# Optimization experiments

Measured on AMD Instinct MI355X. Metric: run time of the kernel, lower is better.

The kernel has to match this reference:

```python
import jax, jax.numpy as jnp
import numpy as np

BN_EPS = 1e-5

def setup_inputs() -> dict:
    key = jax.random.key(0)
    ks = jax.random.split(key, 16)
    B, n, m, C1, C2 = 16, 4096, 1024, 128, 256
    Cin, H1, H2 = C1 + C2, 256, 128  # mlp = [384, 256, 128]
    inp = {
        "unknown": jax.random.normal(ks[0], (B, n, 3), jnp.float32),
        "known": jax.random.normal(ks[1], (B, m, 3), jnp.float32),
        "unknow_feats": jax.random.normal(ks[2], (B, n, C1), jnp.float32),
        "known_feats": jax.random.normal(ks[3], (B, m, C2), jnp.float32),
        # layer 1: 1x1 conv (Cin->H1) + BN (eval stats) + ReLU
        "W1": jax.random.normal(ks[4], (H1, Cin), jnp.float32) * 0.05,
        "b1": jnp.zeros((H1,), jnp.float32),
        "g1": jnp.ones((H1,), jnp.float32),
        "bt1": jnp.zeros((H1,), jnp.float32),
        "mu1": jax.random.normal(ks[5], (H1,), jnp.float32) * 0.1,
        "v1": jax.random.uniform(ks[6], (H1,), jnp.float32, 0.5, 1.5),
        # layer 2: 1x1 conv (H1->H2) + BN + ReLU
        "W2": jax.random.normal(ks[7], (H2, H1), jnp.float32) * 0.05,
        "b2": jnp.zeros((H2,), jnp.float32),
        "g2": jnp.ones((H2,), jnp.float32),
        "bt2": jnp.zeros((H2,), jnp.float32),
        "mu2": jax.random.normal(ks[8], (H2,), jnp.float32) * 0.1,
        "v2": jax.random.uniform(ks[9], (H2,), jnp.float32, 0.5, 1.5),
    }
    return inp

def _fp_forward(unknown, known, unknow_feats, known_feats,
                W1, b1, g1, bt1, mu1, v1,
                W2, b2, g2, bt2, mu2, v2):
    # --- three_nn: brute-force k=3 nearest neighbors (squared distances) ---
    # d2: (B, n, m)
    d2 = jnp.sum((unknown[:, :, None, :] - known[:, None, :, :]) ** 2, axis=-1)
    neg_dist, idx = jax.lax.top_k(-d2, 3)          # (B, n, 3)
    dist = -neg_dist + 1e-10
    dist_recip = 1.0 / dist
    weight = dist_recip / jnp.sum(dist_recip, axis=2, keepdims=True)  # (B, n, 3)
    # --- three_interpolate: inverse-distance weighted gather ---
    feats_nn = jax.vmap(lambda f, i: f[i])(known_feats, idx)  # (B, n, 3, C2)
    interpolated = jnp.einsum('bnkc,bnk->bnc', feats_nn, weight)
    x = jnp.concatenate([interpolated, unknow_feats], axis=-1)  # (B, n, C1+C2)
    # --- SharedMLP: 1x1 conv + BN(eval) + ReLU, twice ---
    for (W, b, g, bt, mu, v) in ((W1, b1, g1, bt1, mu1, v1),
                                 (W2, b2, g2, bt2, mu2, v2)):
        x = jnp.einsum('bnc,oc->bno', x, W) + b
        x = (x - mu) * (g * jax.lax.rsqrt(v + BN_EPS)) + bt
        x = jax.nn.relu(x)
    return x  # (B, n, mlp[-1])

def reference(unknown, known, unknow_feats, known_feats,
              W1, b1, g1, bt1, mu1, v1,
              W2, b2, g2, bt2, mu2, v2):
    return _fp_forward(unknown, known, unknow_feats, known_feats,
                       W1, b1, g1, bt1, mu1, v1,
                       W2, b2, g2, bt2, mu2, v2)
```

## Files before the change

### kernel.cpp

```cpp
#include <hip/hip_runtime.h>

typedef float f32x4 __attribute__((ext_vector_type(4)));
typedef __bf16 bf16x8 __attribute__((ext_vector_type(8)));

#define BN_EPS 1e-5f

__device__ __forceinline__ unsigned short f2bf(float x) {
  union { float f; unsigned u; } v; v.f = x;
  unsigned r = v.u + 0x7fffu + ((v.u >> 16) & 1u);
  return (unsigned short)(r >> 16);
}

__global__ void prep_kernel(const float* __restrict__ W1, const float* __restrict__ b1,
                            const float* __restrict__ g1, const float* __restrict__ bt1,
                            const float* __restrict__ mu1, const float* __restrict__ v1,
                            const float* __restrict__ W2, const float* __restrict__ b2,
                            const float* __restrict__ g2, const float* __restrict__ bt2,
                            const float* __restrict__ mu2, const float* __restrict__ v2,
                            unsigned short* __restrict__ W1b, unsigned short* __restrict__ W2b,
                            float* __restrict__ bias1, float* __restrict__ bias2) {
  int tid = blockIdx.x * 256 + threadIdx.x;
  if (tid < 98304) {
    int o = tid / 384;
    float s = g1[o] * rsqrtf(v1[o] + BN_EPS);
    W1b[tid] = f2bf(W1[tid] * s);
    if (tid < 256) bias1[tid] = (b1[tid] - mu1[tid]) * (g1[tid] * rsqrtf(v1[tid] + BN_EPS)) + bt1[tid];
  } else if (tid < 98304 + 32768) {
    int t = tid - 98304;
    int o = t / 256;
    float s = g2[o] * rsqrtf(v2[o] + BN_EPS);
    W2b[t] = f2bf(W2[t] * s);
    if (t < 128) bias2[t] = (b2[t] - mu2[t]) * (g2[t] * rsqrtf(v2[t] + BN_EPS)) + bt2[t];
  }
}

__global__ __launch_bounds__(256, 2)
void fp_fused_kernel(const float* __restrict__ unknown, const float* __restrict__ known,
                     const float* __restrict__ unknow_feats, const float* __restrict__ known_feats,
                     const unsigned short* __restrict__ W1b, const unsigned short* __restrict__ W2b,
                     const float* __restrict__ bias1, const float* __restrict__ bias2,
                     float* __restrict__ out) {
  __shared__ float kxyz[3072];
  __shared__ float sd[64 * 12];
  __shared__ int   si[64 * 12];
  __shared__ float w_s[64 * 3];
  __shared__ int   i_s[64 * 3];
  __shared__ __align__(16) unsigned char xbuf[64 * 768];

  int bid = blockIdx.x;
  int swz = ((bid & 7) << 7) | (bid >> 3);
  int b   = swz >> 6;
  int i0  = (swz & 63) << 6;

  int tid = threadIdx.x;
  int l = tid & 63;
  int q = tid >> 6;

  for (int t = tid; t < 3072; t += 256) kxyz[t] = known[b * 3072 + t];

  int pi = i0 + l;
  float ux = unknown[(b * 4096 + pi) * 3 + 0];
  float uy = unknown[(b * 4096 + pi) * 3 + 1];
  float uz = unknown[(b * 4096 + pi) * 3 + 2];
  __syncthreads();

  float d0 = 3.0e38f, d1 = 3.0e38f, d2 = 3.0e38f;
  int   j0 = 0, j1 = 0, j2 = 0;
  int jbase = q << 8;
  for (int jj = 0; jj < 256; ++jj) {
    int j = jbase + jj;
    float dx = ux - kxyz[j * 3 + 0];
    float dy = uy - kxyz[j * 3 + 1];
    float dz = uz - kxyz[j * 3 + 2];
    float d = dx * dx + dy * dy + dz * dz;
    bool c2 = d < d2, c1 = d < d1, c0 = d < d0;
    d2 = c1 ? d1 : (c2 ? d : d2);  j2 = c1 ? j1 : (c2 ? j : j2);
    d1 = c0 ? d0 : (c1 ? d : d1);  j1 = c0 ? j0 : (c1 ? j : j1);
    d0 = c0 ? d : d0;              j0 = c0 ? j : j0;
  }
  int sb = l * 12 + q * 3;
  sd[sb] = d0; sd[sb + 1] = d1; sd[sb + 2] = d2;
  si[sb] = j0; si[sb + 1] = j1; si[sb + 2] = j2;
  __syncthreads();

  if (tid < 64) {
    float m0 = 3.0e38f, m1 = 3.0e38f, m2 = 3.0e38f;
    int   n0 = 0, n1 = 0, n2 = 0;
    for (int e = 0; e < 12; ++e) {
      float d = sd[tid * 12 + e]; int j = si[tid * 12 + e];
      bool c2 = d < m2, c1 = d < m1, c0 = d < m0;
      m2 = c1 ? m1 : (c2 ? d : m2);  n2 = c1 ? n1 : (c2 ? j : n2);
      m1 = c0 ? m0 : (c1 ? d : m1);  n1 = c0 ? n0 : (c1 ? j : n1);
      m0 = c0 ? d : m0;              n0 = c0 ? j : n0;
    }
    float r0 = 1.0f / (m0 + 1e-10f);
    float r1 = 1.0f / (m1 + 1e-10f);
    float r2 = 1.0f / (m2 + 1e-10f);
    float rs = 1.0f / (r0 + r1 + r2);
    w_s[tid * 3 + 0] = r0 * rs; i_s[tid * 3 + 0] = n0;
    w_s[tid * 3 + 1] = r1 * rs; i_s[tid * 3 + 1] = n1;
    w_s[tid * 3 + 2] = r2 * rs; i_s[tid * 3 + 2] = n2;
  }
  __syncthreads();

  {
    int pp = tid >> 6;
    int cq = tid & 63;
    const float4* kf = (const float4*)(known_feats + (size_t)b * 1024 * 256);
    for (int po = 0; po < 16; ++po) {
      int p = po * 4 + pp;
      int ia = i_s[p * 3 + 0], ib = i_s[p * 3 + 1], ic = i_s[p * 3 + 2];
      float wa = w_s[p * 3 + 0], wb = w_s[p * 3 + 1], wc = w_s[p * 3 + 2];
      float4 va = kf[ia * 64 + cq];
      float4 vb = kf[ib * 64 + cq];
      float4 vc = kf[ic * 64 + cq];
      ushort4 h;
      h.x = f2bf(wa * va.x + wb * vb.x + wc * vc.x);
      h.y = f2bf(wa * va.y + wb * vb.y + wc * vc.y);
      h.z = f2bf(wa * va.z + wb * vb.z + wc * vc.z);
      h.w = f2bf(wa * va.w + wb * vb.w + wc * vc.w);
      int byte = p * 768 + cq * 8;
      byte ^= (p & 7) << 4;
      *(ushort4*)(xbuf + byte) = h;
    }
  }
  {
    int pp = tid >> 5;
    int cq = tid & 31;
    const float4* uf = (const float4*)(unknow_feats + ((size_t)b * 4096 + i0) * 128);
    for (int po = 0; po < 8; ++po) {
      int p = po * 8 + pp;
      float4 v = uf[p * 32 + cq];
      ushort4 h;
      h.x = f2bf(v.x); h.y = f2bf(v.y); h.z = f2bf(v.z); h.w = f2bf(v.w);
      int byte = p * 768 + 512 + cq * 8;
      byte ^= (p & 7) << 4;
      *(ushort4*)(xbuf + byte) = h;
    }
  }
  __syncthreads();

  int lr = l & 15;
  int lk = l >> 4;
  f32x4 acc[4][4];
  #pragma unroll
  for (int m = 0; m < 4; ++m)
    #pragma unroll
    for (int n = 0; n < 4; ++n) acc[m][n] = (f32x4){0.f, 0.f, 0.f, 0.f};

  for (int kk = 0; kk < 12; ++kk) {
    int kb = kk * 32 + lk * 8;
    bf16x8 a[4];
    #pragma unroll
    for (int m = 0; m < 4; ++m) {
      int row = m * 16 + lr;
      int byte = row * 768 + kb * 2;
      byte ^= (row & 7) << 4;
      a[m] = *(const bf16x8*)(xbuf + byte);
    }
    #pragma unroll
    for (int n = 0; n < 4; ++n) {
      int wr = q * 64 + n * 16 + lr;
      bf16x8 bb = *(const bf16x8*)(W1b + wr * 384 + kb);
      #pragma unroll
      for (int m = 0; m < 4; ++m)
        acc[m][n] = __builtin_amdgcn_mfma_f32_16x16x32_bf16(a[m], bb, acc[m][n], 0, 0, 0);
    }
  }

  float bs1[4];
  #pragma unroll
  for (int n = 0; n < 4; ++n) bs1[n] = bias1[q * 64 + n * 16 + lr];

  __syncthreads();
  #pragma unroll
  for (int m = 0; m < 4; ++m)
    #pragma unroll
    for (int n = 0; n < 4; ++n)
      #pragma unroll
      for (int i = 0; i < 4; ++i) {
        int r = m * 16 + lk * 4 + i;
        int c = q * 64 + n * 16 + lr;
        float val = fmaxf(acc[m][n][i] + bs1[n], 0.0f);
        int byte = r * 512 + c * 2;
        byte ^= (r & 7) << 4;
        *(unsigned short*)(xbuf + byte) = f2bf(val);
      }
  __syncthreads();

  f32x4 acc2[4][2];
  #pragma unroll
  for (int m = 0; m < 4; ++m)
    #pragma unroll
    for (int n = 0; n < 2; ++n) acc2[m][n] = (f32x4){0.f, 0.f, 0.f, 0.f};

  for (int kk = 0; kk < 8; ++kk) {
    int kb = kk * 32 + lk * 8;
    bf16x8 a[4];
    #pragma unroll
    for (int m = 0; m < 4; ++m) {
      int row = m * 16 + lr;
      int byte = row * 512 + kb * 2;
      byte ^= (row & 7) << 4;
      a[m] = *(const bf16x8*)(xbuf + byte);
    }
    #pragma unroll
    for (int n = 0; n < 2; ++n) {
      int wr = q * 32 + n * 16 + lr;
      bf16x8 bb = *(const bf16x8*)(W2b + wr * 256 + kb);
      #pragma unroll
      for (int m = 0; m < 4; ++m)
        acc2[m][n] = __builtin_amdgcn_mfma_f32_16x16x32_bf16(a[m], bb, acc2[m][n], 0, 0, 0);
    }
  }

  float bs2[2];
  #pragma unroll
  for (int n = 0; n < 2; ++n) bs2[n] = bias2[q * 32 + n * 16 + lr];

  float* outb = out + ((size_t)b * 4096 + i0) * 128;
  #pragma unroll
  for (int m = 0; m < 4; ++m)
    #pragma unroll
    for (int n = 0; n < 2; ++n)
      #pragma unroll
      for (int i = 0; i < 4; ++i) {
        int r = m * 16 + lk * 4 + i;
        int c = q * 32 + n * 16 + lr;
        outb[r * 128 + c] = fmaxf(acc2[m][n][i] + bs2[n], 0.0f);
      }
}

extern "C" void kernel_launch(void* const* d_in, const int* in_sizes, int n_in,
                              void* d_out, int out_size, void* d_ws, size_t ws_size,
                              hipStream_t stream) {
  const float* unknown      = (const float*)d_in[0];
  const float* known        = (const float*)d_in[1];
  const float* unknow_feats = (const float*)d_in[2];
  const float* known_feats  = (const float*)d_in[3];
  const float* W1  = (const float*)d_in[4];
  const float* b1  = (const float*)d_in[5];
  const float* g1  = (const float*)d_in[6];
  const float* bt1 = (const float*)d_in[7];
  const float* mu1 = (const float*)d_in[8];
  const float* v1  = (const float*)d_in[9];
  const float* W2  = (const float*)d_in[10];
  const float* b2  = (const float*)d_in[11];
  const float* g2  = (const float*)d_in[12];
  const float* bt2 = (const float*)d_in[13];
  const float* mu2 = (const float*)d_in[14];
  const float* v2  = (const float*)d_in[15];

  unsigned short* W1b = (unsigned short*)d_ws;
  unsigned short* W2b = W1b + 98304;
  float* bias1 = (float*)(W2b + 32768);
  float* bias2 = bias1 + 256;

  prep_kernel<<<512, 256, 0, stream>>>(W1, b1, g1, bt1, mu1, v1,
                                       W2, b2, g2, bt2, mu2, v2,
                                       W1b, W2b, bias1, bias2);
  fp_fused_kernel<<<1024, 256, 0, stream>>>(unknown, known, unknow_feats, known_feats,
                                            W1b, W2b, bias1, bias2, (float*)d_out);
}
```

Measured before the change: 87.66 us.

## Split fused kernel into separate 3-NN and MLP kernels with tuned occupancy

Splits the fused kernel in two. The first kernel computes the 3 nearest neighbours, with each thread handling two query points, float4-padded known coordinates and fmed3-based top-3 updates. It writes the weights plus packed indices to a workspace buffer. The second kernel runs the interpolation and MLP at a higher occupancy target, raises wave priority around the MFMA loops, and stages output through LDS for coalesced float4 stores. This trades an extra launch and a global round trip of the neighbour data for lower LDS/register pressure per kernel and better throughput in each phase.

```diff
diff --git a/kernel.cpp b/kernel.cpp
--- a/kernel.cpp
+++ b/kernel.cpp
@@ -34,18 +34,12 @@
   }
 }
 
-__global__ __launch_bounds__(256, 2)
-void fp_fused_kernel(const float* __restrict__ unknown, const float* __restrict__ known,
-                     const float* __restrict__ unknow_feats, const float* __restrict__ known_feats,
-                     const unsigned short* __restrict__ W1b, const unsigned short* __restrict__ W2b,
-                     const float* __restrict__ bias1, const float* __restrict__ bias2,
-                     float* __restrict__ out) {
-  __shared__ float kxyz[3072];
-  __shared__ float sd[64 * 12];
-  __shared__ int   si[64 * 12];
-  __shared__ float w_s[64 * 3];
-  __shared__ int   i_s[64 * 3];
-  __shared__ __align__(16) unsigned char xbuf[64 * 768];
+__global__ __launch_bounds__(256, 4)
+void nn3_kernel(const float* __restrict__ unknown, const float* __restrict__ known,
+                float4* __restrict__ wi4) {
+  __shared__ float4 kxyz[1024];
+  __shared__ float sd[64 * 25];
+  __shared__ int   si[64 * 25];
 
   int bid = blockIdx.x;
   int swz = ((bid & 7) << 7) | (bid >> 3);
@@ -53,53 +47,113 @@
   int i0  = (swz & 63) << 6;
 
   int tid = threadIdx.x;
-  int l = tid & 63;
-  int q = tid >> 6;
-
-  for (int t = tid; t < 3072; t += 256) kxyz[t] = known[b * 3072 + t];
-
-  int pi = i0 + l;
-  float ux = unknown[(b * 4096 + pi) * 3 + 0];
-  float uy = unknown[(b * 4096 + pi) * 3 + 1];
-  float uz = unknown[(b * 4096 + pi) * 3 + 2];
-  __syncthreads();
-
-  float d0 = 3.0e38f, d1 = 3.0e38f, d2 = 3.0e38f;
-  int   j0 = 0, j1 = 0, j2 = 0;
-  int jbase = q << 8;
-  for (int jj = 0; jj < 256; ++jj) {
-    int j = jbase + jj;
-    float dx = ux - kxyz[j * 3 + 0];
-    float dy = uy - kxyz[j * 3 + 1];
-    float dz = uz - kxyz[j * 3 + 2];
-    float d = dx * dx + dy * dy + dz * dz;
-    bool c2 = d < d2, c1 = d < d1, c0 = d < d0;
-    d2 = c1 ? d1 : (c2 ? d : d2);  j2 = c1 ? j1 : (c2 ? j : j2);
-    d1 = c0 ? d0 : (c1 ? d : d1);  j1 = c0 ? j0 : (c1 ? j : j1);
-    d0 = c0 ? d : d0;              j0 = c0 ? j : j0;
-  }
-  int sb = l * 12 + q * 3;
-  sd[sb] = d0; sd[sb + 1] = d1; sd[sb + 2] = d2;
-  si[sb] = j0; si[sb + 1] = j1; si[sb + 2] = j2;
+
+  float* kf = (float*)kxyz;
+  for (int t = tid; t < 3072; t += 256) {
+    int r = t / 3, c = t - r * 3;
+    kf[r * 4 + c] = known[b * 3072 + t];
+  }
+
+  int u = tid & 31;
+  int q = tid >> 5;
+  int p0 = i0 + u * 2;
+  const float* up = unknown + ((size_t)b * 4096 + p0) * 3;
+  float ax = up[0], ay = up[1], az = up[2];
+  float bx = up[3], by = up[4], bz = up[5];
+  __syncthreads();
+
+  float a0 = 3e38f, a1 = 3e38f, a2 = 3e38f;
+  float e0 = 3e38f, e1 = 3e38f, e2 = 3e38f;
+  int aj0 = 0, aj1 = 0, aj2 = 0, ej0 = 0, ej1 = 0, ej2 = 0;
+  int jb = q << 7;
+  #pragma unroll 4
+  for (int jj = 0; jj < 128; ++jj) {
+    int j = jb + jj;
+    float4 k = kxyz[j];
+    {
+      float dx = ax - k.x, dy = ay - k.y, dz = az - k.z;
+      float d = dx * dx + dy * dy + dz * dz;
+      bool c0 = d < a0, c1 = d < a1, c2 = d < a2;
+      aj2 = c1 ? aj1 : (c2 ? j : aj2);
+      aj1 = c0 ? aj0 : (c1 ? j : aj1);
+      aj0 = c0 ? j : aj0;
+      float na2 = __builtin_amdgcn_fmed3f(a1, a2, d);
+      float na1 = __builtin_amdgcn_fmed3f(a0, a1, d);
+      a0 = fminf(a0, d); a1 = na1; a2 = na2;
+    }
+    {
+      float dx = bx - k.x, dy = by - k.y, dz = bz - k.z;
+      float d = dx * dx + dy * dy + dz * dz;
+      bool c0 = d < e0, c1 = d < e1, c2 = d < e2;
+      ej2 = c1 ? ej1 : (c2 ? j : ej2);
+      ej1 = c0 ? ej0 : (c1 ? j : ej1);
+      ej0 = c0 ? j : ej0;
+      float na2 = __builtin_amdgcn_fmed3f(e1, e2, d);
+      float na1 = __builtin_amdgcn_fmed3f(e0, e1, d);
+      e0 = fminf(e0, d); e1 = na1; e2 = na2;
+    }
+  }
+  {
+    int base = (u * 2) * 25 + q * 3;
+    sd[base] = a0; sd[base + 1] = a1; sd[base + 2] = a2;
+    si[base] = aj0; si[base + 1] = aj1; si[base + 2] = aj2;
+    base += 25;
+    sd[base] = e0; sd[base + 1] = e1; sd[base + 2] = e2;
+    si[base] = ej0; si[base + 1] = ej1; si[base + 2] = ej2;
+  }
   __syncthreads();
 
   if (tid < 64) {
-    float m0 = 3.0e38f, m1 = 3.0e38f, m2 = 3.0e38f;
-    int   n0 = 0, n1 = 0, n2 = 0;
-    for (int e = 0; e < 12; ++e) {
-      float d = sd[tid * 12 + e]; int j = si[tid * 12 + e];
-      bool c2 = d < m2, c1 = d < m1, c0 = d < m0;
-      m2 = c1 ? m1 : (c2 ? d : m2);  n2 = c1 ? n1 : (c2 ? j : n2);
-      m1 = c0 ? m0 : (c1 ? d : m1);  n1 = c0 ? n0 : (c1 ? j : n1);
-      m0 = c0 ? d : m0;              n0 = c0 ? j : n0;
+    float m0 = 3e38f, m1 = 3e38f, m2 = 3e38f;
+    int n0 = 0, n1 = 0, n2 = 0;
+    int base = tid * 25;
+    for (int e = 0; e < 24; ++e) {
+      float d = sd[base + e]; int j = si[base + e];
+      bool c0 = d < m0, c1 = d < m1, c2 = d < m2;
+      n2 = c1 ? n1 : (c2 ? j : n2);
+      n1 = c0 ? n0 : (c1 ? j : n1);
+      n0 = c0 ? j : n0;
+      float t2 = __builtin_amdgcn_fmed3f(m1, m2, d);
+      float t1 = __builtin_amdgcn_fmed3f(m0, m1, d);
+      m0 = fminf(m0, d); m1 = t1; m2 = t2;
     }
     float r0 = 1.0f / (m0 + 1e-10f);
     float r1 = 1.0f / (m1 + 1e-10f);
     float r2 = 1.0f / (m2 + 1e-10f);
     float rs = 1.0f / (r0 + r1 + r2);
-    w_s[tid * 3 + 0] = r0 * rs; i_s[tid * 3 + 0] = n0;
-    w_s[tid * 3 + 1] = r1 * rs; i_s[tid * 3 + 1] = n1;
-    w_s[tid * 3 + 2] = r2 * rs; i_s[tid * 3 + 2] = n2;
+    float4 o;
+    o.x = r0 * rs; o.y = r1 * rs; o.z = r2 * rs;
+    o.w = __int_as_float(n0 | (n1 << 10) | (n2 << 20));
+    wi4[(size_t)b * 4096 + i0 + tid] = o;
+  }
+}
+
+__global__ __launch_bounds__(256, 3)
+void mlp_kernel(const float4* __restrict__ wi4,
+                const float* __restrict__ unknow_feats, const float* __restrict__ known_feats,
+                const unsigned short* __restrict__ W1b, const unsigned short* __restrict__ W2b,
+                const float* __restrict__ bias1, const float* __restrict__ bias2,
+                float* __restrict__ out) {
+  __shared__ float w_s[64 * 3];
+  __shared__ int   i_s[64 * 3];
+  __shared__ __align__(16) unsigned char xbuf[64 * 768];
+
+  int bid = blockIdx.x;
+  int swz = ((bid & 7) << 7) | (bid >> 3);
+  int b   = swz >> 6;
+  int i0  = (swz & 63) << 6;
+
+  int tid = threadIdx.x;
+  int l = tid & 63;
+  int q = tid >> 6;
+
+  if (tid < 64) {
+    float4 v = wi4[(size_t)b * 4096 + i0 + tid];
+    w_s[tid * 3 + 0] = v.x; w_s[tid * 3 + 1] = v.y; w_s[tid * 3 + 2] = v.z;
+    int pk = __float_as_int(v.w);
+    i_s[tid * 3 + 0] = pk & 1023;
+    i_s[tid * 3 + 1] = (pk >> 10) & 1023;
+    i_s[tid * 3 + 2] = (pk >> 20) & 1023;
   }
   __syncthreads();
 
@@ -148,6 +202,7 @@
     #pragma unroll
     for (int n = 0; n < 4; ++n) acc[m][n] = (f32x4){0.f, 0.f, 0.f, 0.f};
 
+  __builtin_amdgcn_s_setprio(1);
   for (int kk = 0; kk < 12; ++kk) {
     int kb = kk * 32 + lk * 8;
     bf16x8 a[4];
@@ -167,6 +222,7 @@
         acc[m][n] = __builtin_amdgcn_mfma_f32_16x16x32_bf16(a[m], bb, acc[m][n], 0, 0, 0);
     }
   }
+  __builtin_amdgcn_s_setprio(0);
 
   float bs1[4];
   #pragma unroll
@@ -194,6 +250,7 @@
     #pragma unroll
     for (int n = 0; n < 2; ++n) acc2[m][n] = (f32x4){0.f, 0.f, 0.f, 0.f};
 
+  __builtin_amdgcn_s_setprio(1);
   for (int kk = 0; kk < 8; ++kk) {
     int kb = kk * 32 + lk * 8;
     bf16x8 a[4];
@@ -213,12 +270,14 @@
         acc2[m][n] = __builtin_amdgcn_mfma_f32_16x16x32_bf16(a[m], bb, acc2[m][n], 0, 0, 0);
     }
   }
+  __builtin_amdgcn_s_setprio(0);
 
   float bs2[2];
   #pragma unroll
   for (int n = 0; n < 2; ++n) bs2[n] = bias2[q * 32 + n * 16 + lr];
 
-  float* outb = out + ((size_t)b * 4096 + i0) * 128;
+  __syncthreads();
+  float* ot = (float*)xbuf;
   #pragma unroll
   for (int m = 0; m < 4; ++m)
     #pragma unroll
@@ -227,8 +286,18 @@
       for (int i = 0; i < 4; ++i) {
         int r = m * 16 + lk * 4 + i;
         int c = q * 32 + n * 16 + lr;
-        outb[r * 128 + c] = fmaxf(acc2[m][n][i] + bs2[n], 0.0f);
+        ot[r * 132 + c] = fmaxf(acc2[m][n][i] + bs2[n], 0.0f);
       }
+  __syncthreads();
+  {
+    float4* out4 = (float4*)(out + ((size_t)b * 4096 + i0) * 128);
+    for (int t = tid; t < 2048; t += 256) {
+      int pr = t >> 5;
+      int c4 = t & 31;
+      float4 v = *(const float4*)(ot + pr * 132 + c4 * 4);
+      out4[pr * 32 + c4] = v;
+    }
+  }
 }
 
 extern "C" void kernel_launch(void* const* d_in, const int* in_sizes, int n_in,
@@ -255,10 +324,12 @@
   unsigned short* W2b = W1b + 98304;
   float* bias1 = (float*)(W2b + 32768);
   float* bias2 = bias1 + 256;
+  float4* wi4  = (float4*)((char*)d_ws + 263680);
 
   prep_kernel<<<512, 256, 0, stream>>>(W1, b1, g1, bt1, mu1, v1,
                                        W2, b2, g2, bt2, mu2, v2,
                                        W1b, W2b, bias1, bias2);
-  fp_fused_kernel<<<1024, 256, 0, stream>>>(unknown, known, unknow_feats, known_feats,
-                                            W1b, W2b, bias1, bias2, (float*)d_out);
-}
+  nn3_kernel<<<1024, 256, 0, stream>>>(unknown, known, wi4);
+  mlp_kernel<<<1024, 256, 0, stream>>>(wi4, unknow_feats, known_feats,
+                                       W1b, W2b, bias1, bias2, (float*)d_out);
+}
```

New measurement: 102.9 us. 1.17x slower.
